# Kernel optimization log

Measured on AMD Instinct MI355X. Metric: run time of the kernel, lower is better.

Reference implementation:

```python
import jax, jax.numpy as jnp
import numpy as np

D = 1024      # input_dim / hidden_size
H = 16        # n_heads
HD = D // H   # head_size = 64
F = 4096      # mlp_dim
EPS = 1e-6


def setup_inputs() -> dict:
    key = jax.random.key(0)
    ks = jax.random.split(key, 16)
    s = 0.02
    inp = {
        "x": jax.random.normal(ks[0], (4, 2048, D), dtype=jnp.float32),
        # attention params (torch Linear: y = x @ W.T + b; we store W as [out,in])
        "Wq": jax.random.normal(ks[1], (D, D), dtype=jnp.float32) * s,
        "bq": jax.random.normal(ks[2], (D,), dtype=jnp.float32) * s,
        "Wk": jax.random.normal(ks[3], (D, D), dtype=jnp.float32) * s,
        "bk": jax.random.normal(ks[4], (D,), dtype=jnp.float32) * s,
        "Wv": jax.random.normal(ks[5], (D, D), dtype=jnp.float32) * s,
        "bv": jax.random.normal(ks[6], (D,), dtype=jnp.float32) * s,
        "Wo": jax.random.normal(ks[7], (D, D), dtype=jnp.float32) * s,
        "bo": jax.random.normal(ks[8], (D,), dtype=jnp.float32) * s,
        # MLP params
        "W1": jax.random.normal(ks[9], (F, D), dtype=jnp.float32) * s,
        "b1": jax.random.normal(ks[10], (F,), dtype=jnp.float32) * s,
        "W2": jax.random.normal(ks[11], (D, F), dtype=jnp.float32) * s,
        "b2": jax.random.normal(ks[12], (D,), dtype=jnp.float32) * s,
        # LayerNorm params
        "ln1_g": jnp.ones((D,), dtype=jnp.float32),
        "ln1_b": jnp.zeros((D,), dtype=jnp.float32),
        "ln2_g": jnp.ones((D,), dtype=jnp.float32),
        "ln2_b": jnp.zeros((D,), dtype=jnp.float32),
    }
    return inp


def _layernorm(x, g, b):
    mu = jnp.mean(x, axis=-1, keepdims=True)
    var = jnp.mean(jnp.square(x - mu), axis=-1, keepdims=True)
    return (x - mu) * jax.lax.rsqrt(var + EPS) * g + b


def reference(x, Wq, bq, Wk, bk, Wv, bv, Wo, bo, W1, b1, W2, b2,
              ln1_g, ln1_b, ln2_g, ln2_b):
    B, S, _ = x.shape
    h = x
    xn = _layernorm(x, ln1_g, ln1_b)
    # Q/K/V projections -> [B, H, S, HD]
    def split_heads(t):
        return t.reshape(B, S, H, HD).transpose(0, 2, 1, 3)
    q = split_heads(xn @ Wq.T + bq)
    k = split_heads(xn @ Wk.T + bk)
    v = split_heads(xn @ Wv.T + bv)
    scores = jnp.einsum('bhqd,bhkd->bhqk', q, k) / np.sqrt(HD).astype(np.float32)
    probs = jax.nn.softmax(scores, axis=-1)
    ctx = jnp.einsum('bhqk,bhkd->bhqd', probs, v)      # [B,H,S,HD]
    ctx = ctx.transpose(0, 2, 1, 3).reshape(B, S, D)
    attn_out = ctx @ Wo.T + bo
    x = attn_out + h
    h = x
    xn = _layernorm(x, ln2_g, ln2_b)
    y = jax.nn.gelu(xn @ W1.T + b1, approximate=False)  # torch nn.GELU() = exact erf gelu
    y = y @ W2.T + b2
    return y + h
```

## Files before the change

### kernel.cpp

```cpp
#include <hip/hip_runtime.h>
#include <hip/hip_bf16.h>
#include <math.h>

typedef __attribute__((ext_vector_type(8))) short short8;
typedef __attribute__((ext_vector_type(4))) float f32x4;

#define MFMA_BF16 __builtin_amdgcn_mfma_f32_16x16x32_bf16

__device__ __forceinline__ ushort f2bf(float f) {
  union { __hip_bfloat16 h; ushort u; } c;
  c.h = __float2bfloat16(f);
  return c.u;
}
__device__ __forceinline__ uint pack_bf16_ru(float a, float b) {
  uint ua = __builtin_bit_cast(uint, a) + 0x8000u;
  uint ub = __builtin_bit_cast(uint, b) + 0x8000u;
  return (ua >> 16) | (ub & 0xffff0000u);
}
__device__ __forceinline__ void async_cp16(const ushort* g, ushort* l) {
  __builtin_amdgcn_global_load_lds(
      (const __attribute__((address_space(1))) void*)g,
      (__attribute__((address_space(3))) void*)l, 16, 0, 0);
}

__global__ __launch_bounds__(256) void conv_all(
    const float* __restrict__ Wq, const float* __restrict__ Wk,
    const float* __restrict__ Wv, const float* __restrict__ Wo,
    const float* __restrict__ W1, const float* __restrict__ W2,
    const float* __restrict__ bq, const float* __restrict__ bk,
    const float* __restrict__ bv,
    ushort* __restrict__ wqkv, ushort* __restrict__ wo,
    ushort* __restrict__ w1, ushort* __restrict__ w2,
    float* __restrict__ bqkv) {
  int i = blockIdx.x * 256 + threadIdx.x;
  if (i < 3145728) {
    const float* src; ushort* dst; int off;
    if (i < 786432)        {
      dst = wqkv; off = i;
      if (i < 262144)      src = Wq + (size_t)i * 4;
      else if (i < 524288) src = Wk + (size_t)(i - 262144) * 4;
      else                 src = Wv + (size_t)(i - 524288) * 4;
    } else if (i < 1048576) { dst = wo; off = i - 786432;  src = Wo + (size_t)off * 4; }
    else if (i < 2097152)   { dst = w1; off = i - 1048576; src = W1 + (size_t)off * 4; }
    else                    { dst = w2; off = i - 2097152; src = W2 + (size_t)off * 4; }
    float4 v = *(const float4*)src;
    ushort4 o;
    o.x = f2bf(v.x); o.y = f2bf(v.y); o.z = f2bf(v.z); o.w = f2bf(v.w);
    ((ushort4*)dst)[off] = o;
  } else if (i < 3146496) {
    int off = i - 3145728;
    const float* src;
    if (off < 256)      src = bq + (size_t)off * 4;
    else if (off < 512) src = bk + (size_t)(off - 256) * 4;
    else                src = bv + (size_t)(off - 512) * 4;
    ((float4*)bqkv)[off] = *(const float4*)src;
  }
}

__global__ __launch_bounds__(256) void ln_kernel(const float* __restrict__ x,
    const float* __restrict__ g, const float* __restrict__ b,
    ushort* __restrict__ out) {
  const int row = blockIdx.x, t = threadIdx.x;
  float4 v = ((const float4*)(x + (size_t)row * 1024))[t];
  float s  = v.x + v.y + v.z + v.w;
  float ss = v.x*v.x + v.y*v.y + v.z*v.z + v.w*v.w;
  #pragma unroll
  for (int off = 32; off >= 1; off >>= 1) {
    s  += __shfl_xor(s, off);
    ss += __shfl_xor(ss, off);
  }
  __shared__ float red[8];
  int wv = t >> 6, ln = t & 63;
  if (ln == 0) { red[wv] = s; red[4 + wv] = ss; }
  __syncthreads();
  float S  = red[0] + red[1] + red[2] + red[3];
  float SS = red[4] + red[5] + red[6] + red[7];
  float mu  = S * (1.0f/1024.0f);
  float var = SS * (1.0f/1024.0f) - mu*mu;
  float rs  = rsqrtf(var + 1e-6f);
  float4 gv = ((const float4*)g)[t];
  float4 bv = ((const float4*)b)[t];
  ushort4 o;
  o.x = f2bf((v.x-mu)*rs*gv.x + bv.x);
  o.y = f2bf((v.y-mu)*rs*gv.y + bv.y);
  o.z = f2bf((v.z-mu)*rs*gv.z + bv.z);
  o.w = f2bf((v.w-mu)*rs*gv.w + bv.w);
  ((ushort4*)(out + (size_t)row*1024))[t] = o;
}

enum { EPI_QK = 0, EPI_VT = 1, EPI_WO = 2, EPI_GELU = 3, EPI_OUT = 4 };

template <int EPI>
__global__ __launch_bounds__(256) void gemm_kernel(const ushort* __restrict__ A,
    const ushort* __restrict__ Bw, const float* __restrict__ bias,
    const float* __restrict__ res, void* __restrict__ outp,
    void* __restrict__ outp2, int K, int N, float scale) {
  __shared__ ushort As[2][128 * 32];
  __shared__ ushort Bs[2][128 * 32];
  const int t = threadIdx.x;
  const int m0 = blockIdx.x * 128, n0 = blockIdx.y * 128;
  const int lane = t & 63, wave = t >> 6;
  const int col = lane & 15, quad = lane >> 4;
  const int wrow = (wave >> 1) * 64, wcol = (wave & 1) * 64;

  f32x4 acc[4][4];
  #pragma unroll
  for (int i = 0; i < 4; i++)
    #pragma unroll
    for (int j = 0; j < 4; j++)
      acc[i][j] = (f32x4){0.f, 0.f, 0.f, 0.f};

  const int lrow = lane >> 2, lcol = (lane & 3) * 8;
  const ushort* Ag = A  + (size_t)(m0 + wave * 32 + lrow) * K + lcol;
  const ushort* Bg = Bw + (size_t)(n0 + wave * 32 + lrow) * K + lcol;
  const int ldso = (wave * 32) * 32;

  for (int k0 = 0; k0 < K; k0 += 64) {
    __syncthreads();
    #pragma unroll
    for (int c = 0; c < 2; c++) {
      async_cp16(Ag + k0 + c * 32,                  &As[c][ldso]);
      async_cp16(Ag + (size_t)16 * K + k0 + c * 32, &As[c][ldso + 16 * 32]);
      async_cp16(Bg + k0 + c * 32,                  &Bs[c][ldso]);
      async_cp16(Bg + (size_t)16 * K + k0 + c * 32, &Bs[c][ldso + 16 * 32]);
    }
    __syncthreads();
    #pragma unroll
    for (int c = 0; c < 2; c++) {
      short8 af[4], bf[4];
      #pragma unroll
      for (int tm = 0; tm < 4; tm++)
        af[tm] = *(const short8*)&As[c][(wrow + tm * 16 + col) * 32 + quad * 8];
      #pragma unroll
      for (int tn = 0; tn < 4; tn++)
        bf[tn] = *(const short8*)&Bs[c][(wcol + tn * 16 + col) * 32 + quad * 8];
      #pragma unroll
      for (int tm = 0; tm < 4; tm++)
        #pragma unroll
        for (int tn = 0; tn < 4; tn++)
          acc[tm][tn] = MFMA_BF16(af[tm], bf[tn], acc[tm][tn], 0, 0, 0);
    }
  }

  #pragma unroll
  for (int tm = 0; tm < 4; tm++) {
    #pragma unroll
    for (int tn = 0; tn < 4; tn++) {
      const int n = n0 + wcol + tn * 16 + col;
      const float bn = (EPI == EPI_VT) ? 0.f : bias[n];
      #pragma unroll
      for (int r = 0; r < 4; r++) {
        const int m = m0 + wrow + tm * 16 + quad * 4 + r;
        float v = acc[tm][tn][r] + bn;
        if (EPI == EPI_QK) {
          int nl = n & 1023, h = nl >> 6, hd = nl & 63;
          int bb = m >> 11, s2 = m & 2047;
          if (n < 1024)
            ((ushort*)outp)[(((size_t)(bb * 16 + h) * 2048 + s2) * 64) + hd] = f2bf(v * scale);
          else
            ((ushort*)outp2)[(((size_t)(bb * 16 + h) * 2048 + s2) * 64) + hd] = f2bf(v);
        } else if (EPI == EPI_VT) {
          float vv = v + bias[m];
          int h = m >> 6, hd = m & 63, bb = n >> 11, s2 = n & 2047;
          ((ushort*)outp)[((size_t)((bb * 16 + h) * 64 + hd)) * 2048 + s2] = f2bf(vv);
        } else if (EPI == EPI_GELU) {
          float u = v * 0.7978845608028654f * (1.0f + 0.044715f * v * v);
          float e = __builtin_amdgcn_exp2f(u * 2.885390081777927f);
          float th = 1.0f - 2.0f * __builtin_amdgcn_rcpf(e + 1.0f);
          ((ushort*)outp)[(size_t)m * N + n] = f2bf(0.5f * v * (1.0f + th));
        } else {
          ((float*)outp)[(size_t)m * N + n] = v + res[(size_t)m * N + n];
        }
      }
    }
  }
}

__global__ __launch_bounds__(256) void attn_kernel(const ushort* __restrict__ Qb,
    const ushort* __restrict__ Kb, const ushort* __restrict__ Vt,
    ushort* __restrict__ ctx) {
  const int lane = threadIdx.x & 63, wave = threadIdx.x >> 6;
  const int col = lane & 15, quad = lane >> 4;
  const int bx = blockIdx.x;
  const int bh = bx & 63;
  const int qt = bx >> 6;
  const int qbase = qt * 128 + wave * 32;
  const ushort* Qh = Qb + (size_t)bh * 2048 * 64;
  const ushort* Kh = Kb + (size_t)bh * 2048 * 64;
  const ushort* Vh = Vt + (size_t)bh * 64 * 2048;

  short8 qa[2][2];
  #pragma unroll
  for (int qg = 0; qg < 2; qg++) {
    const ushort* Qr = Qh + (size_t)(qbase + qg * 16 + col) * 64 + quad * 8;
    qa[qg][0] = *(const short8*)Qr;
    qa[qg][1] = *(const short8*)(Qr + 32);
  }

  f32x4 Ot[2][4];
  float l_part[2];
  #pragma unroll
  for (int qg = 0; qg < 2; qg++) {
    l_part[qg] = 0.f;
    #pragma unroll
    for (int dt = 0; dt < 4; dt++) Ot[qg][dt] = (f32x4){0.f, 0.f, 0.f, 0.f};
  }

  __shared__ ushort Ks[2][2][64 * 32];
  __shared__ ushort Vs[2][2][64 * 32];
  __shared__ ushort P_lds[4][2][16][64];

  const int lrow = lane >> 2;
  const int srow = wave * 16 + lrow;
  const int lcol = ((lane & 3) ^ ((srow >> 1) & 3)) * 8;
  const ushort* Kg = Kh + (size_t)srow * 64 + lcol;
  const ushort* Vg = Vh + (size_t)srow * 2048 + lcol;
  const int so = (wave * 16) * 32;

  const int kvswz = (col >> 1) & 3;
  const int pswz = col & 7;

  async_cp16(Kg,      &Ks[0][0][so]);
  async_cp16(Kg + 32, &Ks[0][1][so]);
  async_cp16(Vg,      &Vs[0][0][so]);
  async_cp16(Vg + 32, &Vs[0][1][so]);
  __syncthreads();

  int cur = 0;
  for (int kb = 0; kb < 2048; kb += 64) {
    if (kb + 64 < 2048) {
      const int nxt = cur ^ 1;
      async_cp16(Kg + (size_t)(kb + 64) * 64,      &Ks[nxt][0][so]);
      async_cp16(Kg + (size_t)(kb + 64) * 64 + 32, &Ks[nxt][1][so]);
      async_cp16(Vg + (kb + 64),                   &Vs[nxt][0][so]);
      async_cp16(Vg + (kb + 64) + 32,              &Vs[nxt][1][so]);
    }

    short8 kf[4][2], vf[4][2];
    #pragma unroll
    for (int kt = 0; kt < 4; kt++)
      #pragma unroll
      for (int c = 0; c < 2; c++)
        kf[kt][c] = *(const short8*)&Ks[cur][c][(kt * 16 + col) * 32 + (quad ^ kvswz) * 8];
    #pragma unroll
    for (int dt = 0; dt < 4; dt++)
      #pragma unroll
      for (int c = 0; c < 2; c++)
        vf[dt][c] = *(const short8*)&Vs[cur][c][(dt * 16 + col) * 32 + (quad ^ kvswz) * 8];

    #pragma unroll
    for (int qg = 0; qg < 2; qg++) {
      f32x4 s[4];
      __builtin_amdgcn_s_setprio(1);
      #pragma unroll
      for (int kt = 0; kt < 4; kt++) {
        s[kt] = (f32x4){0.f, 0.f, 0.f, 0.f};
        s[kt] = MFMA_BF16(kf[kt][0], qa[qg][0], s[kt], 0, 0, 0);
        s[kt] = MFMA_BF16(kf[kt][1], qa[qg][1], s[kt], 0, 0, 0);
      }
      __builtin_amdgcn_s_setprio(0);
      ushort(*P)[64] = P_lds[wave][qg];
      #pragma unroll
      for (int kt = 0; kt < 4; kt++) {
        float p0 = __builtin_amdgcn_exp2f(s[kt][0]);
        float p1 = __builtin_amdgcn_exp2f(s[kt][1]);
        float p2 = __builtin_amdgcn_exp2f(s[kt][2]);
        float p3 = __builtin_amdgcn_exp2f(s[kt][3]);
        l_part[qg] += (p0 + p1) + (p2 + p3);
        uint2 pk;
        pk.x = pack_bf16_ru(p0, p1);
        pk.y = pack_bf16_ru(p2, p3);
        *(uint2*)&P[col][(((2 * kt + (quad >> 1)) ^ pswz) * 8) + (quad & 1) * 4] = pk;
      }
    }
    #pragma unroll
    for (int qg = 0; qg < 2; qg++) {
      #pragma unroll
      for (int c = 0; c < 2; c++) {
        short8 pf = *(const short8*)&P_lds[wave][qg][col][((4 * c + quad) ^ pswz) * 8];
        __builtin_amdgcn_s_setprio(1);
        #pragma unroll
        for (int dt = 0; dt < 4; dt++)
          Ot[qg][dt] = MFMA_BF16(vf[dt][c], pf, Ot[qg][dt], 0, 0, 0);
        __builtin_amdgcn_s_setprio(0);
      }
    }
    __syncthreads();
    cur ^= 1;
  }

  const int bb = bh >> 4, h = bh & 15;
  #pragma unroll
  for (int qg = 0; qg < 2; qg++) {
    float l = l_part[qg];
    l += __shfl_xor(l, 16);
    l += __shfl_xor(l, 32);
    float inv = __builtin_amdgcn_rcpf(l);
    const int q = qbase + qg * 16 + col;
    size_t base = ((size_t)(bb * 2048 + q)) * 1024 + h * 64;
    #pragma unroll
    for (int dt = 0; dt < 4; dt++) {
      ushort4 o;
      o.x = f2bf(Ot[qg][dt][0] * inv);
      o.y = f2bf(Ot[qg][dt][1] * inv);
      o.z = f2bf(Ot[qg][dt][2] * inv);
      o.w = f2bf(Ot[qg][dt][3] * inv);
      *(ushort4*)&ctx[base + dt * 16 + quad * 4] = o;
    }
  }
}

extern "C" void kernel_launch(void* const* d_in, const int* in_sizes, int n_in,
                              void* d_out, int out_size, void* d_ws, size_t ws_size,
                              hipStream_t stream) {
  const float* x     = (const float*)d_in[0];
  const float* Wq    = (const float*)d_in[1];
  const float* bq    = (const float*)d_in[2];
  const float* Wk    = (const float*)d_in[3];
  const float* bk    = (const float*)d_in[4];
  const float* Wv    = (const float*)d_in[5];
  const float* bv    = (const float*)d_in[6];
  const float* Wo    = (const float*)d_in[7];
  const float* bo    = (const float*)d_in[8];
  const float* W1    = (const float*)d_in[9];
  const float* b1    = (const float*)d_in[10];
  const float* W2    = (const float*)d_in[11];
  const float* b2    = (const float*)d_in[12];
  const float* ln1_g = (const float*)d_in[13];
  const float* ln1_b = (const float*)d_in[14];
  const float* ln2_g = (const float*)d_in[15];
  const float* ln2_b = (const float*)d_in[16];

  const size_t MB = 1ull << 20;
  char* ws = (char*)d_ws;
  ushort* Wqkv_b = (ushort*)(ws + 0 * MB);
  ushort* Wo_b   = (ushort*)(ws + 6 * MB);
  ushort* W1_b   = (ushort*)(ws + 8 * MB);
  ushort* W2_b   = (ushort*)(ws + 16 * MB);
  ushort* xn1    = (ushort*)(ws + 24 * MB);
  ushort* Qb     = (ushort*)(ws + 40 * MB);
  ushort* Kb     = (ushort*)(ws + 56 * MB);
  ushort* Vt     = (ushort*)(ws + 72 * MB);
  ushort* ctxb   = (ushort*)(ws + 88 * MB);
  float*  x2     = (float*)(ws + 104 * MB);
  ushort* xn2    = (ushort*)(ws + 136 * MB);
  ushort* y1     = (ushort*)(ws + 152 * MB);
  float*  bqkv   = (float*)(ws + 152 * MB);

  conv_all<<<12291, 256, 0, stream>>>(Wq, Wk, Wv, Wo, W1, W2, bq, bk, bv,
                                      Wqkv_b, Wo_b, W1_b, W2_b, bqkv);

  ln_kernel<<<8192, 256, 0, stream>>>(x, ln1_g, ln1_b, xn1);

  const float cs = 0.125f * 1.4426950408889634f;
  gemm_kernel<EPI_QK><<<dim3(64, 16), 256, 0, stream>>>(
      xn1, Wqkv_b, bqkv, nullptr, Qb, Kb, 1024, 2048, cs);
  gemm_kernel<EPI_VT><<<dim3(8, 64), 256, 0, stream>>>(
      Wqkv_b + (size_t)2048 * 1024, xn1, bqkv + 2048, nullptr, Vt, nullptr,
      1024, 8192, 1.0f);

  attn_kernel<<<1024, 256, 0, stream>>>(Qb, Kb, Vt, ctxb);

  gemm_kernel<EPI_WO><<<dim3(64, 8), 256, 0, stream>>>(
      ctxb, Wo_b, bo, x, x2, nullptr, 1024, 1024, 1.0f);

  ln_kernel<<<8192, 256, 0, stream>>>(x2, ln2_g, ln2_b, xn2);

  gemm_kernel<EPI_GELU><<<dim3(64, 32), 256, 0, stream>>>(
      xn2, W1_b, b1, nullptr, y1, nullptr, 1024, 4096, 1.0f);
  gemm_kernel<EPI_OUT><<<dim3(64, 8), 256, 0, stream>>>(
      y1, W2_b, b2, x2, d_out, nullptr, 4096, 1024, 1.0f);
}
```

Measured before the change: 548.7 us.

## Add 256x256-tile GEMM kernel for QK and GELU projections; use hardware bf16 pack

Introduces a 512-thread GEMM kernel with 256x256 output tiles, double-buffered async global-to-LDS loads and XOR-swizzled shared memory. It is used for the fused Q/K projection and the W1+GELU projection. Larger tiles raise operand reuse and reduce global traffic per FLOP, but they increase register and LDS pressure. With 64 KB of LDS per buffer pair, occupancy may drop, and the grids are small (256 and 512 blocks). Separately, attention now packs probabilities to bf16 with v_cvt_pk_bf16_f32 instead of manual round-up bit arithmetic.

```diff
diff --git a/kernel.cpp b/kernel.cpp
--- a/kernel.cpp
+++ b/kernel.cpp
@@ -11,11 +11,6 @@
   union { __hip_bfloat16 h; ushort u; } c;
   c.h = __float2bfloat16(f);
   return c.u;
-}
-__device__ __forceinline__ uint pack_bf16_ru(float a, float b) {
-  uint ua = __builtin_bit_cast(uint, a) + 0x8000u;
-  uint ub = __builtin_bit_cast(uint, b) + 0x8000u;
-  return (ua >> 16) | (ub & 0xffff0000u);
 }
 __device__ __forceinline__ void async_cp16(const ushort* g, ushort* l) {
   __builtin_amdgcn_global_load_lds(
@@ -152,14 +147,7 @@
       for (int r = 0; r < 4; r++) {
         const int m = m0 + wrow + tm * 16 + quad * 4 + r;
         float v = acc[tm][tn][r] + bn;
-        if (EPI == EPI_QK) {
-          int nl = n & 1023, h = nl >> 6, hd = nl & 63;
-          int bb = m >> 11, s2 = m & 2047;
-          if (n < 1024)
-            ((ushort*)outp)[(((size_t)(bb * 16 + h) * 2048 + s2) * 64) + hd] = f2bf(v * scale);
-          else
-            ((ushort*)outp2)[(((size_t)(bb * 16 + h) * 2048 + s2) * 64) + hd] = f2bf(v);
-        } else if (EPI == EPI_VT) {
+        if (EPI == EPI_VT) {
           float vv = v + bias[m];
           int h = m >> 6, hd = m & 63, bb = n >> 11, s2 = n & 2047;
           ((ushort*)outp)[((size_t)((bb * 16 + h) * 64 + hd)) * 2048 + s2] = f2bf(vv);
@@ -170,6 +158,118 @@
           ((ushort*)outp)[(size_t)m * N + n] = f2bf(0.5f * v * (1.0f + th));
         } else {
           ((float*)outp)[(size_t)m * N + n] = v + res[(size_t)m * N + n];
+        }
+      }
+    }
+  }
+}
+
+template <int EPI>
+__global__ __launch_bounds__(512, 2) void gemm256_kernel(const ushort* __restrict__ A,
+    const ushort* __restrict__ Bw, const float* __restrict__ bias,
+    void* __restrict__ outp, void* __restrict__ outp2, int K, int N, float scale) {
+  __shared__ ushort As[2][256 * 64];
+  __shared__ ushort Bs[2][256 * 64];
+  const int t = threadIdx.x;
+  const int lane = t & 63, wave = t >> 6;
+  const int col = lane & 15, quad = lane >> 4;
+  const int m0 = blockIdx.x * 256, n0 = blockIdx.y * 256;
+  const int wm = wave >> 2, wn = wave & 3;
+
+  f32x4 acc[8][4];
+  #pragma unroll
+  for (int i = 0; i < 8; i++)
+    #pragma unroll
+    for (int j = 0; j < 4; j++)
+      acc[i][j] = (f32x4){0.f, 0.f, 0.f, 0.f};
+
+  size_t aoff[4], boff[4];
+  int sdst[4];
+  #pragma unroll
+  for (int i = 0; i < 4; i++) {
+    int c = i * 512 + t;
+    int row = c >> 3, p = c & 7;
+    int gcol = (p ^ (row & 7)) * 8;
+    aoff[i] = (size_t)(m0 + row) * K + gcol;
+    boff[i] = (size_t)(n0 + row) * K + gcol;
+    sdst[i] = c * 8;
+  }
+
+  const int NT = K >> 6;
+  #pragma unroll
+  for (int i = 0; i < 4; i++) {
+    async_cp16(A  + aoff[i], &As[0][sdst[i]]);
+    async_cp16(Bw + boff[i], &Bs[0][sdst[i]]);
+  }
+
+  int cur = 0;
+  for (int kt = 0; kt < NT; kt++) {
+    if (kt + 1 < NT) {
+      const int nxt = cur ^ 1;
+      const int ko = (kt + 1) << 6;
+      #pragma unroll
+      for (int i = 0; i < 4; i++) {
+        async_cp16(A  + aoff[i] + ko, &As[nxt][sdst[i]]);
+        async_cp16(Bw + boff[i] + ko, &Bs[nxt][sdst[i]]);
+      }
+      asm volatile("s_waitcnt vmcnt(8)" ::: "memory");
+    } else {
+      asm volatile("s_waitcnt vmcnt(0)" ::: "memory");
+    }
+    __builtin_amdgcn_sched_barrier(0);
+    __builtin_amdgcn_s_barrier();
+    __builtin_amdgcn_sched_barrier(0);
+
+    #pragma unroll
+    for (int c = 0; c < 2; c++) {
+      short8 af[8], bf[4];
+      #pragma unroll
+      for (int tm = 0; tm < 8; tm++) {
+        const int row = wm * 128 + tm * 16 + col;
+        af[tm] = *(const short8*)&As[cur][row * 64 + ((c * 4 + quad) ^ (row & 7)) * 8];
+      }
+      #pragma unroll
+      for (int tn = 0; tn < 4; tn++) {
+        const int row = wn * 64 + tn * 16 + col;
+        bf[tn] = *(const short8*)&Bs[cur][row * 64 + ((c * 4 + quad) ^ (row & 7)) * 8];
+      }
+      __builtin_amdgcn_s_setprio(1);
+      #pragma unroll
+      for (int tm = 0; tm < 8; tm++)
+        #pragma unroll
+        for (int tn = 0; tn < 4; tn++)
+          acc[tm][tn] = MFMA_BF16(af[tm], bf[tn], acc[tm][tn], 0, 0, 0);
+      __builtin_amdgcn_s_setprio(0);
+    }
+
+    asm volatile("s_waitcnt lgkmcnt(0)" ::: "memory");
+    __builtin_amdgcn_sched_barrier(0);
+    __builtin_amdgcn_s_barrier();
+    cur ^= 1;
+  }
+
+  #pragma unroll
+  for (int tm = 0; tm < 8; tm++) {
+    #pragma unroll
+    for (int tn = 0; tn < 4; tn++) {
+      const int n = n0 + wn * 64 + tn * 16 + col;
+      const float bn = bias[n];
+      #pragma unroll
+      for (int r = 0; r < 4; r++) {
+        const int m = m0 + wm * 128 + tm * 16 + quad * 4 + r;
+        float v = acc[tm][tn][r] + bn;
+        if (EPI == EPI_QK) {
+          int nl = n & 1023, h = nl >> 6, hd = nl & 63;
+          int bb = m >> 11, s2 = m & 2047;
+          if (n < 1024)
+            ((ushort*)outp)[(((size_t)(bb * 16 + h) * 2048 + s2) * 64) + hd] = f2bf(v * scale);
+          else
+            ((ushort*)outp2)[(((size_t)(bb * 16 + h) * 2048 + s2) * 64) + hd] = f2bf(v);
+        } else {
+          float u = v * 0.7978845608028654f * (1.0f + 0.044715f * v * v);
+          float e = __builtin_amdgcn_exp2f(u * 2.885390081777927f);
+          float th = 1.0f - 2.0f * __builtin_amdgcn_rcpf(e + 1.0f);
+          ((ushort*)outp)[(size_t)m * N + n] = f2bf(0.5f * v * (1.0f + th));
         }
       }
     }
@@ -268,8 +368,8 @@
         float p3 = __builtin_amdgcn_exp2f(s[kt][3]);
         l_part[qg] += (p0 + p1) + (p2 + p3);
         uint2 pk;
-        pk.x = pack_bf16_ru(p0, p1);
-        pk.y = pack_bf16_ru(p2, p3);
+        asm("v_cvt_pk_bf16_f32 %0, %1, %2" : "=v"(pk.x) : "v"(p0), "v"(p1));
+        asm("v_cvt_pk_bf16_f32 %0, %1, %2" : "=v"(pk.y) : "v"(p2), "v"(p3));
         *(uint2*)&P[col][(((2 * kt + (quad >> 1)) ^ pswz) * 8) + (quad & 1) * 4] = pk;
       }
     }
@@ -353,8 +453,8 @@
   ln_kernel<<<8192, 256, 0, stream>>>(x, ln1_g, ln1_b, xn1);
 
   const float cs = 0.125f * 1.4426950408889634f;
-  gemm_kernel<EPI_QK><<<dim3(64, 16), 256, 0, stream>>>(
-      xn1, Wqkv_b, bqkv, nullptr, Qb, Kb, 1024, 2048, cs);
+  gemm256_kernel<EPI_QK><<<dim3(32, 8), 512, 0, stream>>>(
+      xn1, Wqkv_b, bqkv, Qb, Kb, 1024, 2048, cs);
   gemm_kernel<EPI_VT><<<dim3(8, 64), 256, 0, stream>>>(
       Wqkv_b + (size_t)2048 * 1024, xn1, bqkv + 2048, nullptr, Vt, nullptr,
       1024, 8192, 1.0f);
@@ -366,8 +466,8 @@
 
   ln_kernel<<<8192, 256, 0, stream>>>(x2, ln2_g, ln2_b, xn2);
 
-  gemm_kernel<EPI_GELU><<<dim3(64, 32), 256, 0, stream>>>(
-      xn2, W1_b, b1, nullptr, y1, nullptr, 1024, 4096, 1.0f);
+  gemm256_kernel<EPI_GELU><<<dim3(32, 16), 512, 0, stream>>>(
+      xn2, W1_b, b1, y1, nullptr, 1024, 4096, 1.0f);
   gemm_kernel<EPI_OUT><<<dim3(64, 8), 256, 0, stream>>>(
       y1, W2_b, b2, x2, d_out, nullptr, 4096, 1024, 1.0f);
 }
```

Result: faster. 515.2 us (-6.1%).

## Replace GEMM with 512-thread 4-stage pipelined kernel and tune attention P packing

Applied to the files above, without the earlier changes.

Replaces the double-synchronized GEMM with a 512-thread kernel that uses 256-wide N tiles, a templated M tile and a 4-buffer LDS ring. Loads run two K-steps ahead, waits are explicit vmcnt counts, and there is one barrier per step. It also adds an XOR swizzle on LDS rows to avoid bank conflicts and retunes all launch grids. In attention, the P tile is now produced and consumed per query group, which halves P LDS, and P is packed with the hardware v_cvt_pk_bf16_f32 instruction instead of manual rounding. Risks include higher register pressure from larger per-wave accumulators and a slightly different bf16 rounding mode.

```diff
diff --git a/kernel.cpp b/kernel.cpp
--- a/kernel.cpp
+++ b/kernel.cpp
@@ -11,11 +11,6 @@
   union { __hip_bfloat16 h; ushort u; } c;
   c.h = __float2bfloat16(f);
   return c.u;
-}
-__device__ __forceinline__ uint pack_bf16_ru(float a, float b) {
-  uint ua = __builtin_bit_cast(uint, a) + 0x8000u;
-  uint ub = __builtin_bit_cast(uint, b) + 0x8000u;
-  return (ua >> 16) | (ub & 0xffff0000u);
 }
 __device__ __forceinline__ void async_cp16(const ushort* g, ushort* l) {
   __builtin_amdgcn_global_load_lds(
@@ -90,86 +85,124 @@
 
 enum { EPI_QK = 0, EPI_VT = 1, EPI_WO = 2, EPI_GELU = 3, EPI_OUT = 4 };
 
-template <int EPI>
-__global__ __launch_bounds__(256) void gemm_kernel(const ushort* __restrict__ A,
+template <int EPI, int MR>
+__global__ __launch_bounds__(512, 2) void gemm_pipe(const ushort* __restrict__ A,
     const ushort* __restrict__ Bw, const float* __restrict__ bias,
     const float* __restrict__ res, void* __restrict__ outp,
     void* __restrict__ outp2, int K, int N, float scale) {
-  __shared__ ushort As[2][128 * 32];
-  __shared__ ushort Bs[2][128 * 32];
+  constexpr int BM  = 32 * MR;
+  constexpr int ACH = (BM * 4) / 512;
+  constexpr int LPS = ACH + 2;
+  __shared__ ushort As[4][BM * 32];
+  __shared__ ushort Bs[4][256 * 32];
   const int t = threadIdx.x;
-  const int m0 = blockIdx.x * 128, n0 = blockIdx.y * 128;
   const int lane = t & 63, wave = t >> 6;
   const int col = lane & 15, quad = lane >> 4;
-  const int wrow = (wave >> 1) * 64, wcol = (wave & 1) * 64;
-
-  f32x4 acc[4][4];
-  #pragma unroll
-  for (int i = 0; i < 4; i++)
-    #pragma unroll
-    for (int j = 0; j < 4; j++)
-      acc[i][j] = (f32x4){0.f, 0.f, 0.f, 0.f};
-
-  const int lrow = lane >> 2, lcol = (lane & 3) * 8;
-  const ushort* Ag = A  + (size_t)(m0 + wave * 32 + lrow) * K + lcol;
-  const ushort* Bg = Bw + (size_t)(n0 + wave * 32 + lrow) * K + lcol;
-  const int ldso = (wave * 32) * 32;
-
-  for (int k0 = 0; k0 < K; k0 += 64) {
-    __syncthreads();
-    #pragma unroll
-    for (int c = 0; c < 2; c++) {
-      async_cp16(Ag + k0 + c * 32,                  &As[c][ldso]);
-      async_cp16(Ag + (size_t)16 * K + k0 + c * 32, &As[c][ldso + 16 * 32]);
-      async_cp16(Bg + k0 + c * 32,                  &Bs[c][ldso]);
-      async_cp16(Bg + (size_t)16 * K + k0 + c * 32, &Bs[c][ldso + 16 * 32]);
-    }
-    __syncthreads();
-    #pragma unroll
-    for (int c = 0; c < 2; c++) {
-      short8 af[4], bf[4];
-      #pragma unroll
-      for (int tm = 0; tm < 4; tm++)
-        af[tm] = *(const short8*)&As[c][(wrow + tm * 16 + col) * 32 + quad * 8];
+  const int m0 = blockIdx.x * BM, n0 = blockIdx.y * 256;
+  const int wm = wave >> 2, wn = wave & 3;
+
+  f32x4 acc[MR][4];
+  #pragma unroll
+  for (int i = 0; i < MR; i++)
+    #pragma unroll
+    for (int j = 0; j < 4; j++) acc[i][j] = (f32x4){0.f, 0.f, 0.f, 0.f};
+
+  size_t aoff[ACH]; int adst[ACH];
+  size_t boff[2];   int bdst[2];
+  #pragma unroll
+  for (int i = 0; i < ACH; i++) {
+    int c = i * 512 + t, row = c >> 2, p = c & 3;
+    aoff[i] = (size_t)(m0 + row) * K + (p ^ (row & 3)) * 8;
+    adst[i] = c * 8;
+  }
+  #pragma unroll
+  for (int i = 0; i < 2; i++) {
+    int c = i * 512 + t, row = c >> 2, p = c & 3;
+    boff[i] = (size_t)(n0 + row) * K + (p ^ (row & 3)) * 8;
+    bdst[i] = c * 8;
+  }
+
+  const int NT = K >> 5;
+  #pragma unroll
+  for (int i = 0; i < ACH; i++) async_cp16(A + aoff[i], &As[0][adst[i]]);
+  #pragma unroll
+  for (int i = 0; i < 2;  i++) async_cp16(Bw + boff[i], &Bs[0][bdst[i]]);
+  #pragma unroll
+  for (int i = 0; i < ACH; i++) async_cp16(A + aoff[i] + 32, &As[1][adst[i]]);
+  #pragma unroll
+  for (int i = 0; i < 2;  i++) async_cp16(Bw + boff[i] + 32, &Bs[1][bdst[i]]);
+  asm volatile("s_waitcnt vmcnt(%0)" :: "n"(LPS) : "memory");
+  __builtin_amdgcn_sched_barrier(0);
+  __builtin_amdgcn_s_barrier();
+  __builtin_amdgcn_sched_barrier(0);
+
+  for (int j = 0; j < NT; j++) {
+    const int buf = j & 3;
+    if (j + 2 < NT) {
+      const int nb = (j + 2) & 3;
+      const int ko = (j + 2) << 5;
+      #pragma unroll
+      for (int i = 0; i < ACH; i++) async_cp16(A + aoff[i] + ko, &As[nb][adst[i]]);
+      #pragma unroll
+      for (int i = 0; i < 2;  i++) async_cp16(Bw + boff[i] + ko, &Bs[nb][bdst[i]]);
+    }
+    short8 af[MR], bf[4];
+    #pragma unroll
+    for (int tm = 0; tm < MR; tm++) {
+      const int row = wm * (16 * MR) + tm * 16 + col;
+      af[tm] = *(const short8*)&As[buf][row * 32 + (quad ^ (row & 3)) * 8];
+    }
+    #pragma unroll
+    for (int tn = 0; tn < 4; tn++) {
+      const int row = wn * 64 + tn * 16 + col;
+      bf[tn] = *(const short8*)&Bs[buf][row * 32 + (quad ^ (row & 3)) * 8];
+    }
+    __builtin_amdgcn_s_setprio(1);
+    #pragma unroll
+    for (int tm = 0; tm < MR; tm++)
       #pragma unroll
       for (int tn = 0; tn < 4; tn++)
-        bf[tn] = *(const short8*)&Bs[c][(wcol + tn * 16 + col) * 32 + quad * 8];
-      #pragma unroll
-      for (int tm = 0; tm < 4; tm++)
-        #pragma unroll
-        for (int tn = 0; tn < 4; tn++)
-          acc[tm][tn] = MFMA_BF16(af[tm], bf[tn], acc[tm][tn], 0, 0, 0);
-    }
-  }
-
-  #pragma unroll
-  for (int tm = 0; tm < 4; tm++) {
+        acc[tm][tn] = MFMA_BF16(af[tm], bf[tn], acc[tm][tn], 0, 0, 0);
+    __builtin_amdgcn_s_setprio(0);
+    if (j + 2 < NT) {
+      asm volatile("s_waitcnt vmcnt(%0)" :: "n"(LPS) : "memory");
+    } else {
+      asm volatile("s_waitcnt vmcnt(0)" ::: "memory");
+    }
+    __builtin_amdgcn_sched_barrier(0);
+    __builtin_amdgcn_s_barrier();
+    __builtin_amdgcn_sched_barrier(0);
+  }
+
+  #pragma unroll
+  for (int tm = 0; tm < MR; tm++) {
     #pragma unroll
     for (int tn = 0; tn < 4; tn++) {
-      const int n = n0 + wcol + tn * 16 + col;
-      const float bn = (EPI == EPI_VT) ? 0.f : bias[n];
+      const int n = n0 + wn * 64 + tn * 16 + col;
       #pragma unroll
       for (int r = 0; r < 4; r++) {
-        const int m = m0 + wrow + tm * 16 + quad * 4 + r;
-        float v = acc[tm][tn][r] + bn;
+        const int m = m0 + wm * (16 * MR) + tm * 16 + quad * 4 + r;
+        float v = acc[tm][tn][r];
         if (EPI == EPI_QK) {
+          v += bias[n];
           int nl = n & 1023, h = nl >> 6, hd = nl & 63;
           int bb = m >> 11, s2 = m & 2047;
           if (n < 1024)
             ((ushort*)outp)[(((size_t)(bb * 16 + h) * 2048 + s2) * 64) + hd] = f2bf(v * scale);
           else
             ((ushort*)outp2)[(((size_t)(bb * 16 + h) * 2048 + s2) * 64) + hd] = f2bf(v);
+        } else if (EPI == EPI_GELU) {
+          v += bias[n];
+          float u = v * 0.7978845608028654f * (1.0f + 0.044715f * v * v);
+          float e = __builtin_amdgcn_exp2f(u * 2.885390081777927f);
+          float th = 1.0f - 2.0f * __builtin_amdgcn_rcpf(e + 1.0f);
+          ((ushort*)outp)[(size_t)m * N + n] = f2bf(0.5f * v * (1.0f + th));
         } else if (EPI == EPI_VT) {
           float vv = v + bias[m];
           int h = m >> 6, hd = m & 63, bb = n >> 11, s2 = n & 2047;
           ((ushort*)outp)[((size_t)((bb * 16 + h) * 64 + hd)) * 2048 + s2] = f2bf(vv);
-        } else if (EPI == EPI_GELU) {
-          float u = v * 0.7978845608028654f * (1.0f + 0.044715f * v * v);
-          float e = __builtin_amdgcn_exp2f(u * 2.885390081777927f);
-          float th = 1.0f - 2.0f * __builtin_amdgcn_rcpf(e + 1.0f);
-          ((ushort*)outp)[(size_t)m * N + n] = f2bf(0.5f * v * (1.0f + th));
         } else {
-          ((float*)outp)[(size_t)m * N + n] = v + res[(size_t)m * N + n];
+          ((float*)outp)[(size_t)m * N + n] = v + bias[n] + res[(size_t)m * N + n];
         }
       }
     }
@@ -208,7 +241,7 @@
 
   __shared__ ushort Ks[2][2][64 * 32];
   __shared__ ushort Vs[2][2][64 * 32];
-  __shared__ ushort P_lds[4][2][16][64];
+  __shared__ ushort P_lds[4][16][64];
 
   const int lrow = lane >> 2;
   const int srow = wave * 16 + lrow;
@@ -259,7 +292,7 @@
         s[kt] = MFMA_BF16(kf[kt][1], qa[qg][1], s[kt], 0, 0, 0);
       }
       __builtin_amdgcn_s_setprio(0);
-      ushort(*P)[64] = P_lds[wave][qg];
+      ushort(*P)[64] = P_lds[wave];
       #pragma unroll
       for (int kt = 0; kt < 4; kt++) {
         float p0 = __builtin_amdgcn_exp2f(s[kt][0]);
@@ -268,16 +301,13 @@
         float p3 = __builtin_amdgcn_exp2f(s[kt][3]);
         l_part[qg] += (p0 + p1) + (p2 + p3);
         uint2 pk;
-        pk.x = pack_bf16_ru(p0, p1);
-        pk.y = pack_bf16_ru(p2, p3);
+        asm("v_cvt_pk_bf16_f32 %0, %1, %2" : "=v"(pk.x) : "v"(p0), "v"(p1));
+        asm("v_cvt_pk_bf16_f32 %0, %1, %2" : "=v"(pk.y) : "v"(p2), "v"(p3));
         *(uint2*)&P[col][(((2 * kt + (quad >> 1)) ^ pswz) * 8) + (quad & 1) * 4] = pk;
       }
-    }
-    #pragma unroll
-    for (int qg = 0; qg < 2; qg++) {
       #pragma unroll
       for (int c = 0; c < 2; c++) {
-        short8 pf = *(const short8*)&P_lds[wave][qg][col][((4 * c + quad) ^ pswz) * 8];
+        short8 pf = *(const short8*)&P_lds[wave][col][((4 * c + quad) ^ pswz) * 8];
         __builtin_amdgcn_s_setprio(1);
         #pragma unroll
         for (int dt = 0; dt < 4; dt++)
@@ -353,21 +383,21 @@
   ln_kernel<<<8192, 256, 0, stream>>>(x, ln1_g, ln1_b, xn1);
 
   const float cs = 0.125f * 1.4426950408889634f;
-  gemm_kernel<EPI_QK><<<dim3(64, 16), 256, 0, stream>>>(
+  gemm_pipe<EPI_QK, 8><<<dim3(32, 8), 512, 0, stream>>>(
       xn1, Wqkv_b, bqkv, nullptr, Qb, Kb, 1024, 2048, cs);
-  gemm_kernel<EPI_VT><<<dim3(8, 64), 256, 0, stream>>>(
+  gemm_pipe<EPI_VT, 4><<<dim3(8, 32), 512, 0, stream>>>(
       Wqkv_b + (size_t)2048 * 1024, xn1, bqkv + 2048, nullptr, Vt, nullptr,
       1024, 8192, 1.0f);
 
   attn_kernel<<<1024, 256, 0, stream>>>(Qb, Kb, Vt, ctxb);
 
-  gemm_kernel<EPI_WO><<<dim3(64, 8), 256, 0, stream>>>(
+  gemm_pipe<EPI_WO, 4><<<dim3(64, 4), 512, 0, stream>>>(
       ctxb, Wo_b, bo, x, x2, nullptr, 1024, 1024, 1.0f);
 
   ln_kernel<<<8192, 256, 0, stream>>>(x2, ln2_g, ln2_b, xn2);
 
-  gemm_kernel<EPI_GELU><<<dim3(64, 32), 256, 0, stream>>>(
+  gemm_pipe<EPI_GELU, 8><<<dim3(32, 16), 512, 0, stream>>>(
       xn2, W1_b, b1, nullptr, y1, nullptr, 1024, 4096, 1.0f);
-  gemm_kernel<EPI_OUT><<<dim3(64, 8), 256, 0, stream>>>(
+  gemm_pipe<EPI_OUT, 4><<<dim3(64, 4), 512, 0, stream>>>(
       y1, W2_b, b2, x2, d_out, nullptr, 4096, 1024, 1.0f);
 }
```

Result: slower. 578.7 us (+5.5%).
